# Kernel optimization log

Measured on AMD Instinct MI355X. Metric: run time of the kernel, lower is better.

The kernel has to match this reference:

```python
import jax, jax.numpy as jnp
import numpy as np

E = 1024   # embed_size
H = 16     # heads
D = E // H # head_dim = 64
F = 4 * E  # ffn hidden = 4096
N, S = 4, 2048
EPS = 1e-5


def _layernorm(x, w, b):
    m = jnp.mean(x, axis=-1, keepdims=True)
    v = jnp.var(x, axis=-1, keepdims=True)
    return (x - m) * jax.lax.rsqrt(v + EPS) * w + b


def setup_inputs() -> dict:
    key = jax.random.key(0)
    ks = jax.random.split(key, 10)
    s = 0.02
    return {
        "x": jax.random.normal(ks[0], (N, S, E), dtype=jnp.float32),
        "Wq": jax.random.normal(ks[1], (E, E), dtype=jnp.float32) * s,
        "Wk": jax.random.normal(ks[2], (E, E), dtype=jnp.float32) * s,
        "Wv": jax.random.normal(ks[3], (E, E), dtype=jnp.float32) * s,
        "Wo": jax.random.normal(ks[4], (E, E), dtype=jnp.float32) * s,
        "bo": jnp.zeros((E,), dtype=jnp.float32),
        "ln1_w": jnp.ones((E,), dtype=jnp.float32),
        "ln1_b": jnp.zeros((E,), dtype=jnp.float32),
        "ln2_w": jnp.ones((E,), dtype=jnp.float32),
        "ln2_b": jnp.zeros((E,), dtype=jnp.float32),
        "W1": jax.random.normal(ks[5], (F, E), dtype=jnp.float32) * s,
        "bf1": jnp.zeros((F,), dtype=jnp.float32),
        "W2": jax.random.normal(ks[6], (E, F), dtype=jnp.float32) * s,
        "bf2": jnp.zeros((E,), dtype=jnp.float32),
    }


def reference(x, Wq, Wk, Wv, Wo, bo, ln1_w, ln1_b, ln2_w, ln2_b, W1, bf1, W2, bf2):
    n, s, _ = x.shape
    # projections (torch Linear: x @ W.T), no bias for q/k/v
    q = (x @ Wq.T).reshape(n, s, H, D).transpose(0, 2, 1, 3)  # (N,H,S,D)
    k = (x @ Wk.T).reshape(n, s, H, D).transpose(0, 2, 1, 3)
    v = (x @ Wv.T).reshape(n, s, H, D).transpose(0, 2, 1, 3)
    # NOTE: faithful to original einsum strings applied to permuted tensors.
    # energy: (N, H, H, S)
    energy = jnp.einsum('nqhd,nkhd->nqkh', q, k)
    attention = jax.nn.softmax(energy / jnp.sqrt(jnp.float32(D)), axis=3)
    # out: (N, H, S, D); k and v axes each summed independently (as in torch)
    out = jnp.einsum('nqkh,nvhd->nqhd', attention, v).reshape(n, s, E)
    attn = out @ Wo.T + bo
    # residual + LN1 (dropout is identity in eval mode)
    x = _layernorm(attn + x, ln1_w, ln1_b)
    # FFN
    ff = jnp.maximum(x @ W1.T + bf1, 0.0) @ W2.T + bf2
    x = _layernorm(ff + x, ln2_w, ln2_b)
    return x
```

## Files before the change

kernel.cpp:

```cpp
#include <hip/hip_runtime.h>

typedef __attribute__((ext_vector_type(8))) __bf16 bf16x8;
typedef __attribute__((ext_vector_type(8))) unsigned short us8;
typedef __attribute__((ext_vector_type(4))) float f32x4;

#define DEV __device__ __forceinline__

DEV unsigned short f2bf(float f) {
    unsigned u = __builtin_bit_cast(unsigned, f);
    u += 0x7fffu + ((u >> 16) & 1u);
    return (unsigned short)(u >> 16);
}
DEV float bf2f(unsigned short h) {
    return __builtin_bit_cast(float, (unsigned)h << 16);
}

DEV void gload_lds16(const void* g, void* l) {
    __builtin_amdgcn_global_load_lds(
        (const __attribute__((address_space(1))) unsigned int*)g,
        (__attribute__((address_space(3))) unsigned int*)l, 16, 0, 0);
}

#define VMCNT8 asm volatile("s_waitcnt vmcnt(8)" ::: "memory")
#define VMCNT4 asm volatile("s_waitcnt vmcnt(4)" ::: "memory")
#define VMCNT0 asm volatile("s_waitcnt vmcnt(0)" ::: "memory")
#define BAR __builtin_amdgcn_s_barrier()
#define LGKM0                                          \
    asm volatile("s_waitcnt lgkmcnt(0)" ::: "memory"); \
    __builtin_amdgcn_sched_barrier(0)

template <int EPI>
__global__ __launch_bounds__(512) void gemm256(
    const unsigned short* __restrict__ A, const unsigned short* __restrict__ B,
    void* __restrict__ Cv, const float* __restrict__ bias,
    int lda, int ldb, int N, int Kslice) {
    extern __shared__ char smem[];
    const int t = threadIdx.x;

    const int gx = gridDim.x, gy = gridDim.y;
    const int total = gx * gy * gridDim.z;
    int flat = blockIdx.x + gx * (blockIdx.y + gy * blockIdx.z);
    flat = (flat & 7) * (total >> 3) + (flat >> 3);
    const int bx = flat % gx;
    const int byz = flat / gx;
    const int by = byz % gy;
    const int z = byz / gy;

    const int m0 = by * 256, n0 = bx * 256;
    const unsigned short* Ag = A + (size_t)z * Kslice;
    const unsigned short* Bg = B + (size_t)z * Kslice;
    const int NT = Kslice >> 5;

    size_t aoff[2], boff[2];
    int loff[2];
#pragma unroll
    for (int j = 0; j < 2; ++j) {
        int cj = j * 512 + t;
        int row = cj >> 2, slot = cj & 3;
        int col = (slot ^ ((row >> 1) & 3)) << 3;
        aoff[j] = (size_t)(m0 + row) * lda + col;
        boff[j] = (size_t)(n0 + row) * ldb + col;
        loff[j] = cj << 4;
    }

    const int lane = t & 63, r = lane & 15, g = lane >> 4;
    const int wid = t >> 6, wm = wid >> 2, wn = wid & 3;
    const int s0 = (g ^ ((r >> 1) & 3)) << 4;
    const int aRowB = (wm * 128 + r) * 64 + s0;
    const int bRowB = 16384 + (wn * 64 + r) * 64 + s0;

#define LDA8(buf, mi) (*(const bf16x8*)((buf) + aRowB + (mi) * 1024))
#define LDB8(buf, ni) (*(const bf16x8*)((buf) + bRowB + (ni) * 1024))
#define STAGE_A(buf, kt)                                                  \
    do {                                                                  \
        _Pragma("unroll") for (int j = 0; j < 2; ++j)                     \
            gload_lds16(Ag + aoff[j] + (size_t)(kt) * 32, (buf) + loff[j]); \
    } while (0)
#define STAGE_B(buf, kt)                                                  \
    do {                                                                  \
        _Pragma("unroll") for (int j = 0; j < 2; ++j)                     \
            gload_lds16(Bg + boff[j] + (size_t)(kt) * 32,                 \
                        (buf) + 16384 + loff[j]);                         \
    } while (0)

    f32x4 acc[8][4] = {};

    STAGE_A(smem, 0);
    STAGE_B(smem, 0);
    STAGE_A(smem + 32768, 1);
    STAGE_B(smem + 32768, 1);
    STAGE_A(smem + 65536, 2);
    STAGE_B(smem + 65536, 2);

    for (int kt = 0; kt < NT; ++kt) {
        if (kt < NT - 2) {
            VMCNT8;
        } else if (kt == NT - 2) {
            VMCNT4;
        } else {
            VMCNT0;
        }
        BAR;
        char* buf = smem + (kt & 3) * 32768;
        char* nbuf = smem + ((kt + 3) & 3) * 32768;
        const bool st = (kt + 3) < NT;
        bf16x8 bfr[4], af[4];
#pragma unroll
        for (int ni = 0; ni < 4; ++ni) bfr[ni] = LDB8(buf, ni);
#pragma unroll
        for (int q = 0; q < 4; ++q) af[q] = LDA8(buf, q);
        if (st) STAGE_A(nbuf, kt + 3);
        BAR;
        LGKM0;
        __builtin_amdgcn_s_setprio(1);
#pragma unroll
        for (int q = 0; q < 4; ++q)
#pragma unroll
            for (int ni = 0; ni < 4; ++ni)
                acc[q][ni] = __builtin_amdgcn_mfma_f32_16x16x32_bf16(
                    af[q], bfr[ni], acc[q][ni], 0, 0, 0);
        __builtin_amdgcn_s_setprio(0);
#pragma unroll
        for (int q = 0; q < 4; ++q) af[q] = LDA8(buf, 4 + q);
        if (st) STAGE_B(nbuf, kt + 3);
        BAR;
        LGKM0;
        __builtin_amdgcn_s_setprio(1);
#pragma unroll
        for (int q = 0; q < 4; ++q)
#pragma unroll
            for (int ni = 0; ni < 4; ++ni)
                acc[4 + q][ni] = __builtin_amdgcn_mfma_f32_16x16x32_bf16(
                    af[q], bfr[ni], acc[4 + q][ni], 0, 0, 0);
        __builtin_amdgcn_s_setprio(0);
    }

    const int crow0 = m0 + wm * 128 + g * 4;
    const int ccol0 = n0 + wn * 64 + r;
    float* Cp = (float*)Cv + (size_t)gridDim.y * 256 * N * z;
#pragma unroll
    for (int mi = 0; mi < 8; ++mi) {
#pragma unroll
        for (int ni = 0; ni < 4; ++ni) {
            int col = ccol0 + ni * 16;
            float bval = (EPI == 2) ? bias[col] : 0.f;
#pragma unroll
            for (int j = 0; j < 4; ++j) {
                int row = crow0 + mi * 16 + j;
                float v = acc[mi][ni][j];
                if (EPI == 0) {
                    ((unsigned short*)Cv)[(size_t)row * N + col] = f2bf(v);
                } else if (EPI == 1) {
                    Cp[(size_t)row * N + col] = v;
                } else {
                    v = fmaxf(v + bval, 0.f);
                    ((unsigned short*)Cv)[(size_t)row * N + col] = f2bf(v);
                }
            }
        }
    }
#undef LDA8
#undef LDB8
#undef STAGE_A
#undef STAGE_B
}

__global__ __launch_bounds__(256) void cvt_kernel(
    const float* __restrict__ in, unsigned short* __restrict__ out, int n4) {
    int idx = blockIdx.x * 256 + threadIdx.x;
    if (idx >= n4) return;
    float4 v = *(const float4*)(in + (size_t)idx * 4);
    ushort4 u = make_ushort4(f2bf(v.x), f2bf(v.y), f2bf(v.z), f2bf(v.w));
    *(ushort4*)(out + (size_t)idx * 4) = u;
}

__global__ __launch_bounds__(256) void energy_kernel(
    const unsigned short* __restrict__ QKV, float* __restrict__ E) {
    __shared__ __attribute__((aligned(16))) unsigned short Qs[8 * 1024];
    __shared__ __attribute__((aligned(16))) unsigned short Ks[8 * 1024];
    const int tid = threadIdx.x;
    const int n = blockIdx.y;
    const int s0 = blockIdx.x * 8;
#pragma unroll
    for (int c = 0; c < 4; ++c) {
        int e = c * 2048 + tid * 8;
        int row = e >> 10, col = e & 1023;
        int jj = col >> 6, db = (col >> 3) & 7;
        int sw = jj * 64 + (((db + jj) & 7) << 3);
        size_t gbase = (size_t)(n * 2048 + s0 + row) * 3072;
        *(us8*)(Qs + row * 1024 + sw) = *(const us8*)(QKV + gbase + col);
        *(us8*)(Ks + row * 1024 + sw) = *(const us8*)(QKV + gbase + 1024 + col);
    }
    __syncthreads();
    const int i = tid >> 4, j = tid & 15;
#pragma unroll
    for (int s = 0; s < 8; ++s) {
        float acc = 0.f;
#pragma unroll
        for (int d8 = 0; d8 < 8; ++d8) {
            us8 q = *(const us8*)(Qs + s * 1024 + i * 64 + (((d8 + i) & 7) << 3));
            us8 k = *(const us8*)(Ks + s * 1024 + j * 64 + (((d8 + j) & 7) << 3));
#pragma unroll
            for (int t = 0; t < 8; ++t) acc += bf2f(q[t]) * bf2f(k[t]);
        }
        E[(size_t)(n * 2048 + s0 + s) * 256 + tid] = acc * 0.125f;
    }
}

__global__ __launch_bounds__(256) void smax_part(
    const float* __restrict__ E, float* __restrict__ Mp, float* __restrict__ Zp) {
    const int p = threadIdx.x, n = blockIdx.y, sc = blockIdx.x;
    float m = -1e30f, z = 0.f;
    const float* base = E + ((size_t)n * 2048 + sc * 128) * 256 + p;
    for (int s = 0; s < 128; ++s) {
        float e = base[(size_t)s * 256];
        float mn = fmaxf(m, e);
        z = z * __expf(m - mn) + __expf(e - mn);
        m = mn;
    }
    int idx = (n * 16 + sc) * 256 + p;
    Mp[idx] = m;
    Zp[idx] = z;
}

__global__ __launch_bounds__(256) void smax_fin(
    const float* __restrict__ Mp, const float* __restrict__ Zp,
    float* __restrict__ Mf, float* __restrict__ RZf) {
    const int p = threadIdx.x, n = blockIdx.x;
    float m = -1e30f;
    for (int c = 0; c < 16; ++c) m = fmaxf(m, Mp[(n * 16 + c) * 256 + p]);
    float z = 0.f;
    for (int c = 0; c < 16; ++c)
        z += Zp[(n * 16 + c) * 256 + p] * __expf(Mp[(n * 16 + c) * 256 + p] - m);
    Mf[n * 256 + p] = m;
    RZf[n * 256 + p] = 1.f / z;
}

__global__ __launch_bounds__(256) void attnsrc_kernel(
    const unsigned short* __restrict__ QKV, const float* __restrict__ E,
    const float* __restrict__ Mf, const float* __restrict__ RZf,
    unsigned short* __restrict__ ASRC) {
    const int lane = threadIdx.x & 63;
    const int widx = blockIdx.x * 4 + (threadIdx.x >> 6);
    const int n = widx >> 11, s = widx & 2047;
    float vs = 0.f;
    const unsigned short* vrow = QKV + (size_t)(n * 2048 + s) * 3072 + 2048;
#pragma unroll
    for (int h = 0; h < 16; ++h) vs += bf2f(vrow[h * 64 + lane]);
    float aval = 0.f;
    if (lane < 16) {
        const float* erow = E + (size_t)(n * 2048 + s) * 256 + lane * 16;
        const float* mrow = Mf + n * 256 + lane * 16;
        const float* zrow = RZf + n * 256 + lane * 16;
#pragma unroll
        for (int j = 0; j < 16; ++j)
            aval += __expf(erow[j] - mrow[j]) * zrow[j];
    }
#pragma unroll
    for (int h = 0; h < 16; ++h) {
        float ah = __shfl(aval, h, 64);
        size_t row = (size_t)n * 2048 + h * 128 + (s >> 4);
        ASRC[row * 1024 + (s & 15) * 64 + lane] = f2bf(ah * vs);
    }
}

__global__ __launch_bounds__(256) void ln_kernel(
    const float* __restrict__ lin, const float* __restrict__ lin2,
    const float* __restrict__ bias, const float* __restrict__ resid,
    const float* __restrict__ w, const float* __restrict__ b,
    unsigned short* __restrict__ obf, float* __restrict__ of) {
    __shared__ float sm[16];
    const int row = blockIdx.x, c = threadIdx.x * 4;
    const size_t off = (size_t)row * 1024 + c;
    float4 v = *(const float4*)(lin + off);
    float4 bs = *(const float4*)(bias + c);
    float4 rx = *(const float4*)(resid + off);
    float t0 = v.x + bs.x + rx.x;
    float t1 = v.y + bs.y + rx.y;
    float t2 = v.z + bs.z + rx.z;
    float t3 = v.w + bs.w + rx.w;
    if (lin2) {
        float4 v2 = *(const float4*)(lin2 + off);
        t0 += v2.x; t1 += v2.y; t2 += v2.z; t3 += v2.w;
    }
    float s = t0 + t1 + t2 + t3;
    float ss = t0 * t0 + t1 * t1 + t2 * t2 + t3 * t3;
#pragma unroll
    for (int o = 32; o > 0; o >>= 1) {
        s += __shfl_down(s, o, 64);
        ss += __shfl_down(ss, o, 64);
    }
    const int wv = threadIdx.x >> 6, ln = threadIdx.x & 63;
    if (ln == 0) {
        sm[wv] = s;
        sm[8 + wv] = ss;
    }
    __syncthreads();
    if (threadIdx.x == 0) {
        sm[4] = sm[0] + sm[1] + sm[2] + sm[3];
        sm[12] = sm[8] + sm[9] + sm[10] + sm[11];
    }
    __syncthreads();
    s = sm[4];
    ss = sm[12];
    float mean = s * (1.f / 1024.f);
    float var = ss * (1.f / 1024.f) - mean * mean;
    float rstd = rsqrtf(var + 1e-5f);
    float4 wv4 = *(const float4*)(w + c);
    float4 bv4 = *(const float4*)(b + c);
    float o0 = (t0 - mean) * rstd * wv4.x + bv4.x;
    float o1 = (t1 - mean) * rstd * wv4.y + bv4.y;
    float o2 = (t2 - mean) * rstd * wv4.z + bv4.z;
    float o3 = (t3 - mean) * rstd * wv4.w + bv4.w;
    if (of) {
        float4 o = make_float4(o0, o1, o2, o3);
        *(float4*)(of + off) = o;
    }
    if (obf) {
        ushort4 u = make_ushort4(f2bf(o0), f2bf(o1), f2bf(o2), f2bf(o3));
        *(ushort4*)(obf + off) = u;
    }
}

extern "C" void kernel_launch(void* const* d_in, const int* in_sizes, int n_in,
                              void* d_out, int out_size, void* d_ws, size_t ws_size,
                              hipStream_t stream) {
    const float* x = (const float*)d_in[0];
    const float* Wq = (const float*)d_in[1];
    const float* Wk = (const float*)d_in[2];
    const float* Wv = (const float*)d_in[3];
    const float* Wo = (const float*)d_in[4];
    const float* bo = (const float*)d_in[5];
    const float* ln1w = (const float*)d_in[6];
    const float* ln1b = (const float*)d_in[7];
    const float* ln2w = (const float*)d_in[8];
    const float* ln2b = (const float*)d_in[9];
    const float* W1 = (const float*)d_in[10];
    const float* bf1 = (const float*)d_in[11];
    const float* W2 = (const float*)d_in[12];
    const float* bf2 = (const float*)d_in[13];

    char* ws = (char*)d_ws;
    const size_t MB = 1u << 20;
    unsigned short* W1bf = (unsigned short*)(ws + 0);
    unsigned short* W2bf = (unsigned short*)(ws + 8 * MB);
    unsigned short* Wobf = (unsigned short*)(ws + 16 * MB);
    unsigned short* Wqkvbf = (unsigned short*)(ws + 18 * MB);
    float* Mp = (float*)(ws + 24 * MB);
    float* Zp = (float*)(ws + 24 * MB + 64 * 1024);
    float* Mfin = (float*)(ws + 24 * MB + 128 * 1024);
    float* RZfin = (float*)(ws + 24 * MB + 160 * 1024);
    float* x1f = (float*)(ws + 16 * MB);
    unsigned short* ASRC = (unsigned short*)(ws + 48 * MB);
    unsigned short* x1bf = (unsigned short*)(ws + 48 * MB);
    float* AL = (float*)(ws + 64 * MB);
    unsigned short* H1 = (unsigned short*)(ws + 64 * MB);
    unsigned short* QKV = (unsigned short*)(ws + 128 * MB);
    float* FF = (float*)(ws + 128 * MB);
    unsigned short* xbf = (unsigned short*)(ws + 176 * MB);
    float* EN = (float*)(ws + 176 * MB);

    auto k0 = gemm256<0>; auto k1 = gemm256<1>; auto k2 = gemm256<2>;
    (void)hipFuncSetAttribute((const void*)k0, hipFuncAttributeMaxDynamicSharedMemorySize, 131072);
    (void)hipFuncSetAttribute((const void*)k1, hipFuncAttributeMaxDynamicSharedMemorySize, 131072);
    (void)hipFuncSetAttribute((const void*)k2, hipFuncAttributeMaxDynamicSharedMemorySize, 131072);

    auto cvt = [&](const float* src, unsigned short* dst, int n) {
        int n4 = n >> 2;
        cvt_kernel<<<dim3((n4 + 255) / 256), dim3(256), 0, stream>>>(src, dst, n4);
    };
    cvt(x, xbf, 8192 * 1024);
    cvt(Wq, Wqkvbf, 1024 * 1024);
    cvt(Wk, Wqkvbf + 1024 * 1024, 1024 * 1024);
    cvt(Wv, Wqkvbf + 2 * 1024 * 1024, 1024 * 1024);
    cvt(Wo, Wobf, 1024 * 1024);
    cvt(W1, W1bf, 4096 * 1024);
    cvt(W2, W2bf, 4096 * 1024);

    gemm256<0><<<dim3(12, 32, 1), 512, 131072, stream>>>(
        xbf, Wqkvbf, QKV, nullptr, 1024, 1024, 3072, 1024);
    energy_kernel<<<dim3(256, 4), 256, 0, stream>>>(QKV, EN);
    smax_part<<<dim3(16, 4), 256, 0, stream>>>(EN, Mp, Zp);
    smax_fin<<<dim3(4), 256, 0, stream>>>(Mp, Zp, Mfin, RZfin);
    attnsrc_kernel<<<dim3(2048), 256, 0, stream>>>(QKV, EN, Mfin, RZfin, ASRC);
    gemm256<1><<<dim3(4, 32, 2), 512, 131072, stream>>>(
        ASRC, Wobf, AL, nullptr, 1024, 1024, 1024, 512);
    ln_kernel<<<dim3(8192), 256, 0, stream>>>(
        AL, AL + (size_t)8192 * 1024, bo, x, ln1w, ln1b, x1bf, x1f);
    gemm256<2><<<dim3(16, 32, 1), 512, 131072, stream>>>(
        x1bf, W1bf, H1, bf1, 1024, 1024, 4096, 1024);
    gemm256<1><<<dim3(4, 32, 2), 512, 131072, stream>>>(
        H1, W2bf, FF, nullptr, 4096, 4096, 1024, 2048);
    ln_kernel<<<dim3(8192), 256, 0, stream>>>(
        FF, FF + (size_t)8192 * 1024, bf2, x1f, ln2w, ln2b, nullptr, (float*)d_out);
}
```

Measured before the change: 468.0 us.

## Restructure GEMM to BK=64 double-buffered pipeline, fuse weight casts, use bf16 residuals

The GEMM mainloop moves from a 32-wide K tile with a 4-stage ring to a 64-wide K tile with two buffers, split into four quadrant MFMA phases interleaved with half-tile async loads and barriers. The six weight conversion launches become one fused kernel. Softmax partial reduction gets more chunks for parallelism. The LayerNorm kernels now read bf16 residuals instead of fp32, which cuts traffic but loses residual precision. The extra barriers per K step and the shallower prefetch could expose load latency.

```diff
diff --git a/kernel.cpp b/kernel.cpp
--- a/kernel.cpp
+++ b/kernel.cpp
@@ -21,13 +21,13 @@
         (__attribute__((address_space(3))) unsigned int*)l, 16, 0, 0);
 }
 
-#define VMCNT8 asm volatile("s_waitcnt vmcnt(8)" ::: "memory")
 #define VMCNT4 asm volatile("s_waitcnt vmcnt(4)" ::: "memory")
 #define VMCNT0 asm volatile("s_waitcnt vmcnt(0)" ::: "memory")
-#define BAR __builtin_amdgcn_s_barrier()
-#define LGKM0                                          \
+#define LGKM0S                                         \
     asm volatile("s_waitcnt lgkmcnt(0)" ::: "memory"); \
     __builtin_amdgcn_sched_barrier(0)
+#define BAR __builtin_amdgcn_s_barrier()
+#define SCHED0 __builtin_amdgcn_sched_barrier(0)
 
 template <int EPI>
 __global__ __launch_bounds__(512) void gemm256(
@@ -49,90 +49,116 @@
     const int m0 = by * 256, n0 = bx * 256;
     const unsigned short* Ag = A + (size_t)z * Kslice;
     const unsigned short* Bg = B + (size_t)z * Kslice;
-    const int NT = Kslice >> 5;
+    const int NT = Kslice >> 6;
 
     size_t aoff[2], boff[2];
     int loff[2];
 #pragma unroll
     for (int j = 0; j < 2; ++j) {
-        int cj = j * 512 + t;
-        int row = cj >> 2, slot = cj & 3;
-        int col = (slot ^ ((row >> 1) & 3)) << 3;
-        aoff[j] = (size_t)(m0 + row) * lda + col;
-        boff[j] = (size_t)(n0 + row) * ldb + col;
-        loff[j] = cj << 4;
+        int c = j * 512 + t;
+        int srow = c >> 3;
+        int scol = ((c & 7) ^ (srow & 7)) << 3;
+        aoff[j] = (size_t)(m0 + srow) * lda + scol;
+        boff[j] = (size_t)(n0 + srow) * ldb + scol;
+        loff[j] = c << 4;
     }
 
     const int lane = t & 63, r = lane & 15, g = lane >> 4;
     const int wid = t >> 6, wm = wid >> 2, wn = wid & 3;
-    const int s0 = (g ^ ((r >> 1) & 3)) << 4;
-    const int aRowB = (wm * 128 + r) * 64 + s0;
-    const int bRowB = 16384 + (wn * 64 + r) * 64 + s0;
-
-#define LDA8(buf, mi) (*(const bf16x8*)((buf) + aRowB + (mi) * 1024))
-#define LDB8(buf, ni) (*(const bf16x8*)((buf) + bRowB + (ni) * 1024))
-#define STAGE_A(buf, kt)                                                  \
-    do {                                                                  \
-        _Pragma("unroll") for (int j = 0; j < 2; ++j)                     \
-            gload_lds16(Ag + aoff[j] + (size_t)(kt) * 32, (buf) + loff[j]); \
+    int sA[2];
+    sA[0] = ((0 + g) ^ (r & 7)) << 4;
+    sA[1] = ((4 + g) ^ (r & 7)) << 4;
+    const int aBase = wm * 16384 + r * 128;
+    const int bBase = 32768 + (wn >> 1) * 16384 + ((wn & 1) * 64 + r) * 128;
+
+#define STAGE_A(base, h, kt)                                                  \
+    do {                                                                      \
+        _Pragma("unroll") for (int j = 0; j < 2; ++j)                         \
+            gload_lds16(Ag + aoff[j] + (size_t)(h) * 128 * lda +              \
+                            (size_t)(kt) * 64,                                \
+                        smem + (base) + (h) * 16384 + loff[j]);               \
     } while (0)
-#define STAGE_B(buf, kt)                                                  \
-    do {                                                                  \
-        _Pragma("unroll") for (int j = 0; j < 2; ++j)                     \
-            gload_lds16(Bg + boff[j] + (size_t)(kt) * 32,                 \
-                        (buf) + 16384 + loff[j]);                         \
+#define STAGE_B(base, h, kt)                                                  \
+    do {                                                                      \
+        _Pragma("unroll") for (int j = 0; j < 2; ++j)                         \
+            gload_lds16(Bg + boff[j] + (size_t)(h) * 128 * ldb +              \
+                            (size_t)(kt) * 64,                                \
+                        smem + (base) + 32768 + (h) * 16384 + loff[j]);       \
     } while (0)
 
+#define RD_AF(dbase, qm)                                                      \
+    _Pragma("unroll") for (int mi = 0; mi < 4; ++mi)                          \
+        _Pragma("unroll") for (int kk = 0; kk < 2; ++kk)                      \
+            af[mi][kk] = *(const bf16x8*)(smem + (dbase) + aBase +            \
+                                          ((qm) * 64 + mi * 16) * 128 + sA[kk]);
+#define RD_BF(dbase, qn, BF)                                                  \
+    _Pragma("unroll") for (int ni = 0; ni < 2; ++ni)                          \
+        _Pragma("unroll") for (int kk = 0; kk < 2; ++kk)                      \
+            BF[ni][kk] = *(const bf16x8*)(smem + (dbase) + bBase +            \
+                                          ((qn) * 32 + ni * 16) * 128 + sA[kk]);
+#define MM(qm, qn, BF)                                                        \
+    __builtin_amdgcn_s_setprio(1);                                            \
+    _Pragma("unroll") for (int mi = 0; mi < 4; ++mi)                          \
+        _Pragma("unroll") for (int ni = 0; ni < 2; ++ni)                      \
+            _Pragma("unroll") for (int kk = 0; kk < 2; ++kk)                  \
+                acc[(qm) * 4 + mi][(qn) * 2 + ni] =                           \
+                    __builtin_amdgcn_mfma_f32_16x16x32_bf16(                  \
+                        af[mi][kk], BF[ni][kk],                               \
+                        acc[(qm) * 4 + mi][(qn) * 2 + ni], 0, 0, 0);          \
+    __builtin_amdgcn_s_setprio(0);
+
     f32x4 acc[8][4] = {};
-
-    STAGE_A(smem, 0);
-    STAGE_B(smem, 0);
-    STAGE_A(smem + 32768, 1);
-    STAGE_B(smem + 32768, 1);
-    STAGE_A(smem + 65536, 2);
-    STAGE_B(smem + 65536, 2);
+    bf16x8 af[4][2], bf0[2][2], bf1[2][2];
+
+    STAGE_A(0, 0, 0);
+    STAGE_A(0, 1, 0);
+    STAGE_B(0, 0, 0);
+    STAGE_B(0, 1, 0);
+    if (1 < NT) {
+        STAGE_B(65536, 0, 1);
+        STAGE_B(65536, 1, 1);
+        VMCNT4;
+    } else {
+        VMCNT0;
+    }
+    BAR;
 
     for (int kt = 0; kt < NT; ++kt) {
-        if (kt < NT - 2) {
-            VMCNT8;
-        } else if (kt == NT - 2) {
+        const int dbase = (kt & 1) * 65536;
+        const int nbase = dbase ^ 65536;
+        RD_AF(dbase, 0);
+        RD_BF(dbase, 0, bf0);
+        if (kt + 1 < NT) STAGE_A(nbase, 0, kt + 1);
+        SCHED0;
+        BAR;
+        LGKM0S;
+        MM(0, 0, bf0);
+        BAR;
+        RD_BF(dbase, 1, bf1);
+        if (kt + 1 < NT) STAGE_A(nbase, 1, kt + 1);
+        SCHED0;
+        BAR;
+        LGKM0S;
+        MM(0, 1, bf1);
+        BAR;
+        RD_AF(dbase, 1);
+        if (kt + 2 < NT) STAGE_B(dbase, 0, kt + 2);
+        SCHED0;
+        BAR;
+        LGKM0S;
+        MM(1, 0, bf0);
+        BAR;
+        if (kt + 2 < NT) {
+            STAGE_B(dbase, 1, kt + 2);
             VMCNT4;
         } else {
             VMCNT0;
         }
-        BAR;
-        char* buf = smem + (kt & 3) * 32768;
-        char* nbuf = smem + ((kt + 3) & 3) * 32768;
-        const bool st = (kt + 3) < NT;
-        bf16x8 bfr[4], af[4];
-#pragma unroll
-        for (int ni = 0; ni < 4; ++ni) bfr[ni] = LDB8(buf, ni);
-#pragma unroll
-        for (int q = 0; q < 4; ++q) af[q] = LDA8(buf, q);
-        if (st) STAGE_A(nbuf, kt + 3);
-        BAR;
-        LGKM0;
-        __builtin_amdgcn_s_setprio(1);
-#pragma unroll
-        for (int q = 0; q < 4; ++q)
-#pragma unroll
-            for (int ni = 0; ni < 4; ++ni)
-                acc[q][ni] = __builtin_amdgcn_mfma_f32_16x16x32_bf16(
-                    af[q], bfr[ni], acc[q][ni], 0, 0, 0);
-        __builtin_amdgcn_s_setprio(0);
-#pragma unroll
-        for (int q = 0; q < 4; ++q) af[q] = LDA8(buf, 4 + q);
-        if (st) STAGE_B(nbuf, kt + 3);
-        BAR;
-        LGKM0;
-        __builtin_amdgcn_s_setprio(1);
-#pragma unroll
-        for (int q = 0; q < 4; ++q)
-#pragma unroll
-            for (int ni = 0; ni < 4; ++ni)
-                acc[4 + q][ni] = __builtin_amdgcn_mfma_f32_16x16x32_bf16(
-                    af[q], bfr[ni], acc[4 + q][ni], 0, 0, 0);
-        __builtin_amdgcn_s_setprio(0);
+        SCHED0;
+        BAR;
+        SCHED0;
+        MM(1, 1, bf1);
+        BAR;
     }
 
     const int crow0 = m0 + wm * 128 + g * 4;
@@ -159,10 +185,11 @@
             }
         }
     }
-#undef LDA8
-#undef LDB8
 #undef STAGE_A
 #undef STAGE_B
+#undef RD_AF
+#undef RD_BF
+#undef MM
 }
 
 __global__ __launch_bounds__(256) void cvt_kernel(
@@ -172,6 +199,35 @@
     float4 v = *(const float4*)(in + (size_t)idx * 4);
     ushort4 u = make_ushort4(f2bf(v.x), f2bf(v.y), f2bf(v.z), f2bf(v.w));
     *(ushort4*)(out + (size_t)idx * 4) = u;
+}
+
+__global__ __launch_bounds__(256) void wcvt_kernel(
+    const float* __restrict__ Wq, const float* __restrict__ Wk,
+    const float* __restrict__ Wv, const float* __restrict__ Wo,
+    const float* __restrict__ W1, const float* __restrict__ W2,
+    unsigned short* __restrict__ Wqkvbf, unsigned short* __restrict__ Wobf,
+    unsigned short* __restrict__ W1bf, unsigned short* __restrict__ W2bf) {
+    int idx = blockIdx.x * 256 + threadIdx.x;
+    const float* src;
+    unsigned short* dst;
+    if (idx < 786432) {
+        dst = Wqkvbf + (size_t)idx * 4;
+        src = (idx < 262144)   ? Wq + (size_t)idx * 4
+              : (idx < 524288) ? Wk + (size_t)(idx - 262144) * 4
+                               : Wv + (size_t)(idx - 524288) * 4;
+    } else if (idx < 1048576) {
+        src = Wo + (size_t)(idx - 786432) * 4;
+        dst = Wobf + (size_t)(idx - 786432) * 4;
+    } else if (idx < 2097152) {
+        src = W1 + (size_t)(idx - 1048576) * 4;
+        dst = W1bf + (size_t)(idx - 1048576) * 4;
+    } else {
+        src = W2 + (size_t)(idx - 2097152) * 4;
+        dst = W2bf + (size_t)(idx - 2097152) * 4;
+    }
+    float4 v = *(const float4*)src;
+    ushort4 u = make_ushort4(f2bf(v.x), f2bf(v.y), f2bf(v.z), f2bf(v.w));
+    *(ushort4*)dst = u;
 }
 
 __global__ __launch_bounds__(256) void energy_kernel(
@@ -211,14 +267,14 @@
     const float* __restrict__ E, float* __restrict__ Mp, float* __restrict__ Zp) {
     const int p = threadIdx.x, n = blockIdx.y, sc = blockIdx.x;
     float m = -1e30f, z = 0.f;
-    const float* base = E + ((size_t)n * 2048 + sc * 128) * 256 + p;
-    for (int s = 0; s < 128; ++s) {
+    const float* base = E + ((size_t)n * 2048 + sc * 32) * 256 + p;
+    for (int s = 0; s < 32; ++s) {
         float e = base[(size_t)s * 256];
         float mn = fmaxf(m, e);
         z = z * __expf(m - mn) + __expf(e - mn);
         m = mn;
     }
-    int idx = (n * 16 + sc) * 256 + p;
+    int idx = (n * 64 + sc) * 256 + p;
     Mp[idx] = m;
     Zp[idx] = z;
 }
@@ -228,10 +284,10 @@
     float* __restrict__ Mf, float* __restrict__ RZf) {
     const int p = threadIdx.x, n = blockIdx.x;
     float m = -1e30f;
-    for (int c = 0; c < 16; ++c) m = fmaxf(m, Mp[(n * 16 + c) * 256 + p]);
+    for (int c = 0; c < 64; ++c) m = fmaxf(m, Mp[(n * 64 + c) * 256 + p]);
     float z = 0.f;
-    for (int c = 0; c < 16; ++c)
-        z += Zp[(n * 16 + c) * 256 + p] * __expf(Mp[(n * 16 + c) * 256 + p] - m);
+    for (int c = 0; c < 64; ++c)
+        z += Zp[(n * 64 + c) * 256 + p] * __expf(Mp[(n * 64 + c) * 256 + p] - m);
     Mf[n * 256 + p] = m;
     RZf[n * 256 + p] = 1.f / z;
 }
@@ -266,7 +322,7 @@
 
 __global__ __launch_bounds__(256) void ln_kernel(
     const float* __restrict__ lin, const float* __restrict__ lin2,
-    const float* __restrict__ bias, const float* __restrict__ resid,
+    const float* __restrict__ bias, const unsigned short* __restrict__ residbf,
     const float* __restrict__ w, const float* __restrict__ b,
     unsigned short* __restrict__ obf, float* __restrict__ of) {
     __shared__ float sm[16];
@@ -274,11 +330,11 @@
     const size_t off = (size_t)row * 1024 + c;
     float4 v = *(const float4*)(lin + off);
     float4 bs = *(const float4*)(bias + c);
-    float4 rx = *(const float4*)(resid + off);
-    float t0 = v.x + bs.x + rx.x;
-    float t1 = v.y + bs.y + rx.y;
-    float t2 = v.z + bs.z + rx.z;
-    float t3 = v.w + bs.w + rx.w;
+    ushort4 rx = *(const ushort4*)(residbf + off);
+    float t0 = v.x + bs.x + bf2f(rx.x);
+    float t1 = v.y + bs.y + bf2f(rx.y);
+    float t2 = v.z + bs.z + bf2f(rx.z);
+    float t3 = v.w + bs.w + bf2f(rx.w);
     if (lin2) {
         float4 v2 = *(const float4*)(lin2 + off);
         t0 += v2.x; t1 += v2.y; t2 += v2.z; t3 += v2.w;
@@ -342,15 +398,16 @@
 
     char* ws = (char*)d_ws;
     const size_t MB = 1u << 20;
+    const size_t KB = 1u << 10;
     unsigned short* W1bf = (unsigned short*)(ws + 0);
     unsigned short* W2bf = (unsigned short*)(ws + 8 * MB);
     unsigned short* Wobf = (unsigned short*)(ws + 16 * MB);
     unsigned short* Wqkvbf = (unsigned short*)(ws + 18 * MB);
     float* Mp = (float*)(ws + 24 * MB);
-    float* Zp = (float*)(ws + 24 * MB + 64 * 1024);
-    float* Mfin = (float*)(ws + 24 * MB + 128 * 1024);
-    float* RZfin = (float*)(ws + 24 * MB + 160 * 1024);
-    float* x1f = (float*)(ws + 16 * MB);
+    float* Zp = (float*)(ws + 24 * MB + 256 * KB);
+    float* Mfin = (float*)(ws + 24 * MB + 512 * KB);
+    float* RZfin = (float*)(ws + 24 * MB + 528 * KB);
+    float* EN = (float*)(ws + 32 * MB);
     unsigned short* ASRC = (unsigned short*)(ws + 48 * MB);
     unsigned short* x1bf = (unsigned short*)(ws + 48 * MB);
     float* AL = (float*)(ws + 64 * MB);
@@ -358,39 +415,30 @@
     unsigned short* QKV = (unsigned short*)(ws + 128 * MB);
     float* FF = (float*)(ws + 128 * MB);
     unsigned short* xbf = (unsigned short*)(ws + 176 * MB);
-    float* EN = (float*)(ws + 176 * MB);
 
     auto k0 = gemm256<0>; auto k1 = gemm256<1>; auto k2 = gemm256<2>;
     (void)hipFuncSetAttribute((const void*)k0, hipFuncAttributeMaxDynamicSharedMemorySize, 131072);
     (void)hipFuncSetAttribute((const void*)k1, hipFuncAttributeMaxDynamicSharedMemorySize, 131072);
     (void)hipFuncSetAttribute((const void*)k2, hipFuncAttributeMaxDynamicSharedMemorySize, 131072);
 
-    auto cvt = [&](const float* src, unsigned short* dst, int n) {
-        int n4 = n >> 2;
-        cvt_kernel<<<dim3((n4 + 255) / 256), dim3(256), 0, stream>>>(src, dst, n4);
-    };
-    cvt(x, xbf, 8192 * 1024);
-    cvt(Wq, Wqkvbf, 1024 * 1024);
-    cvt(Wk, Wqkvbf + 1024 * 1024, 1024 * 1024);
-    cvt(Wv, Wqkvbf + 2 * 1024 * 1024, 1024 * 1024);
-    cvt(Wo, Wobf, 1024 * 1024);
-    cvt(W1, W1bf, 4096 * 1024);
-    cvt(W2, W2bf, 4096 * 1024);
+    cvt_kernel<<<dim3(8192), 256, 0, stream>>>(x, xbf, 2097152);
+    wcvt_kernel<<<dim3(12288), 256, 0, stream>>>(Wq, Wk, Wv, Wo, W1, W2,
+                                                 Wqkvbf, Wobf, W1bf, W2bf);
 
     gemm256<0><<<dim3(12, 32, 1), 512, 131072, stream>>>(
         xbf, Wqkvbf, QKV, nullptr, 1024, 1024, 3072, 1024);
     energy_kernel<<<dim3(256, 4), 256, 0, stream>>>(QKV, EN);
-    smax_part<<<dim3(16, 4), 256, 0, stream>>>(EN, Mp, Zp);
+    smax_part<<<dim3(64, 4), 256, 0, stream>>>(EN, Mp, Zp);
     smax_fin<<<dim3(4), 256, 0, stream>>>(Mp, Zp, Mfin, RZfin);
     attnsrc_kernel<<<dim3(2048), 256, 0, stream>>>(QKV, EN, Mfin, RZfin, ASRC);
     gemm256<1><<<dim3(4, 32, 2), 512, 131072, stream>>>(
         ASRC, Wobf, AL, nullptr, 1024, 1024, 1024, 512);
     ln_kernel<<<dim3(8192), 256, 0, stream>>>(
-        AL, AL + (size_t)8192 * 1024, bo, x, ln1w, ln1b, x1bf, x1f);
+        AL, AL + (size_t)8192 * 1024, bo, xbf, ln1w, ln1b, x1bf, nullptr);
     gemm256<2><<<dim3(16, 32, 1), 512, 131072, stream>>>(
         x1bf, W1bf, H1, bf1, 1024, 1024, 4096, 1024);
     gemm256<1><<<dim3(4, 32, 2), 512, 131072, stream>>>(
         H1, W2bf, FF, nullptr, 4096, 4096, 1024, 2048);
     ln_kernel<<<dim3(8192), 256, 0, stream>>>(
-        FF, FF + (size_t)8192 * 1024, bf2, x1f, ln2w, ln2b, nullptr, (float*)d_out);
-}
+        FF, FF + (size_t)8192 * 1024, bf2, x1bf, ln2w, ln2b, nullptr, (float*)d_out);
+}
```

After: 439.3 us. 6.1% less time.
